# Optimization experiments

Hardware: AMD Instinct MI355X
Metric: run time of the kernel (lower is better)

## Reference

```python
import jax, jax.numpy as jnp
import numpy as np

B, C, F, N = 8, 128, 16, 512  # batch, in_channels, frames, num_nodes


def setup_inputs() -> dict:
    key = jax.random.key(0)
    k = jax.random.split(key, 6)
    return {
        # uniform(0,1) -> all entries nonzero -> complete graph with self-loops
        "Y": jax.random.uniform(k[0], (B, F, N, N), dtype=jnp.float32),
        "infos": jax.random.normal(k[1], (B, C, F, N), dtype=jnp.float32),
        # denseLayer: Linear(3C, C) -> weight [C, 3C], bias [C]
        "W_dense": jax.random.normal(k[2], (C, 3 * C), dtype=jnp.float32) / np.sqrt(3 * C).astype(np.float32),
        "b_dense": jax.random.normal(k[3], (C,), dtype=jnp.float32) * 0.01,
        # NodeApplyModule linear: Linear(C, C)
        "W_node": jax.random.normal(k[4], (C, C), dtype=jnp.float32) / np.sqrt(C).astype(np.float32),
        "b_node": jax.random.normal(k[5], (C,), dtype=jnp.float32) * 0.01,
    }


def reference(Y, infos, W_dense, b_dense, W_node, b_node):
    Bs, Cs, Fs, Ns = infos.shape
    # graph_update: frame 0 uses Y[:,0], frames 1..11 use Y[:,1], frames >11 use Y[:,2]
    frames = jnp.arange(Fs)
    y_idx = jnp.where(frames == 0, 0, jnp.where(frames <= 11, 1, 2))
    M = (Y[:, y_idx] != 0).astype(infos.dtype)          # [B,F,N,N] adjacency mask (u->v)
    X = jnp.transpose(infos, (0, 2, 3, 1))               # [B,F,N,C] node features

    # msg(u,v) = X[u] * (cat[X[u], X[v], X[u]-X[v]] @ W_dense.T + b_dense)
    # Linear is separable: gate(u,v) = S[u] + D[v] + b_dense with
    #   S = X @ (W1+W3).T, D = X @ (W2-W3).T
    W1, W2, W3 = jnp.split(W_dense, 3, axis=1)           # each [C,C]
    S = jnp.einsum('bfnc,dc->bfnd', X, W1 + W3)
    D = jnp.einsum('bfnc,dc->bfnd', X, W2 - W3)

    # mean over incoming edges u of msg(u,v):
    #   sum_u M[u,v] * X[u]*S[u]  +  (sum_u M[u,v]*X[u]) * (D[v]+b)
    A1 = jnp.einsum('bfuv,bfuc->bfvc', M, X * S)
    A2 = jnp.einsum('bfuv,bfuc->bfvc', M, X)
    deg = jnp.maximum(M.sum(axis=2), 1.0)[..., None]     # in-degree [B,F,N,1]
    agg = (A1 + A2 * (D + b_dense)) / deg

    # NodeApplyModule: relu(Linear(agg))
    h = jax.nn.relu(jnp.einsum('bfnc,oc->bfno', agg, W_node) + b_node)
    # reshape/permute to [B, C, F, N] and final relu (idempotent after relu)
    return jax.nn.relu(jnp.transpose(h, (0, 3, 1, 2)))
```

## Files before the change

### kernel.cpp

```cpp
#include <hip/hip_runtime.h>

#define B_ 8
#define C_ 128
#define F_ 16
#define N_ 512
#define CAP_ (N_ * N_)

typedef __attribute__((ext_vector_type(8))) short bf16x8;
typedef __attribute__((ext_vector_type(4))) float f32x4;

#define MFMA(a, b, c) __builtin_amdgcn_mfma_f32_16x16x32_bf16((a), (b), (c), 0, 0, 0)
#define SWZ(x) ((x) ^ ((((x) >> 8) & 7) << 4))

__device__ __forceinline__ ushort f2bf(float x) {
    unsigned u = __float_as_uint(x);
    u += 0x7fffu + ((u >> 16) & 1u);
    return (ushort)(u >> 16);
}

__global__ __launch_bounds__(256) void k_wprep(
    const float* __restrict__ Wd, const float* __restrict__ Wn,
    float* __restrict__ Wsum, float* __restrict__ Wdiff, float* __restrict__ WsumT,
    ushort* __restrict__ WdT_bf, float* __restrict__ WnT)
{
    int i = blockIdx.x * 256 + threadIdx.x;
    int d = i >> 7, c = i & 127;
    const float* row = Wd + (size_t)d * (3 * C_);
    float w1 = row[c], w2 = row[C_ + c], w3 = row[2 * C_ + c];
    float ws = w1 + w3, wdf = w2 - w3;
    Wsum[i] = ws;
    Wdiff[i] = wdf;
    WsumT[(size_t)c * C_ + d] = ws;
    WdT_bf[(size_t)c * C_ + d] = f2bf(wdf);
    WnT[i] = Wn[(size_t)(i & 127) * C_ + (i >> 7)];
}

__global__ __launch_bounds__(256) void k_deg(
    const float* __restrict__ Y, float* __restrict__ deg,
    int* __restrict__ cnt, int* __restrict__ list)
{
    __shared__ float red[256];
    int bg = blockIdx.x, vc = blockIdx.y, t = threadIdx.x;
    int b = bg / 3, g = bg % 3;
    int vl = t & 31, q = t >> 5;
    int v = vc * 32 + vl;
    const float* Yp = Y + ((size_t)b * F_ + g) * N_ * N_ + v;
    float dsum = 0.f;
    #pragma unroll 4
    for (int i = 0; i < 64; ++i) {
        int u = q * 64 + i;
        float a = Yp[(size_t)u * N_];
        if (a == 0.f) {
            int idx = atomicAdd(&cnt[bg], 1);
            list[(size_t)bg * CAP_ + idx] = (u << 9) | v;
        } else dsum += 1.f;
    }
    red[t] = dsum;
    __syncthreads();
    if (t < 32) {
        float s = 0.f;
        #pragma unroll
        for (int qq = 0; qq < 8; ++qq) s += red[qq * 32 + t];
        deg[(size_t)bg * N_ + vc * 32 + t] = s;
    }
}

__global__ __launch_bounds__(256) void k_gram(
    const float* __restrict__ infos, const float* __restrict__ WsumT,
    float* __restrict__ A1row, float* __restrict__ A2row)
{
    __shared__ float smf[8448];
    __shared__ float red[256];
    short* Xs = (short*)smf;
    float* Gl = smf;
    int bf = blockIdx.x, nh = blockIdx.y, t = threadIdx.x;
    int b = bf >> 4, f = bf & 15;
    const float* Xg = infos + ((size_t)b * C_ * F_ + f) * N_;

    float a2p0 = 0.f, a2p1 = 0.f, a2p2 = 0.f, a2p3 = 0.f;

    auto STAGE = [&](int buf, int ks) {
        int u0 = ks * 32;
        #pragma unroll
        for (int it = 0; it < 4; ++it) {
            int idx = it * 256 + t;
            int c = idx >> 3, uq = idx & 7;
            const float4 x = *(const float4*)(Xg + (size_t)c * (F_ * N_) + u0 + uq * 4);
            float s4 = x.x + x.y + x.z + x.w;
            if (it == 0) a2p0 += s4; else if (it == 1) a2p1 += s4;
            else if (it == 2) a2p2 += s4; else a2p3 += s4;
            short4 h;
            h.x = (short)f2bf(x.x); h.y = (short)f2bf(x.y);
            h.z = (short)f2bf(x.z); h.w = (short)f2bf(x.w);
            *(short4*)&Xs[buf * 5120 + c * 40 + uq * 4] = h;
        }
    };

    int l = t & 63, w = t >> 6;
    int r = l & 15, q = l >> 4;
    f32x4 acc[2][4];
    #pragma unroll
    for (int mi = 0; mi < 2; ++mi)
        #pragma unroll
        for (int ni = 0; ni < 4; ++ni) acc[mi][ni] = (f32x4){0.f, 0.f, 0.f, 0.f};

    STAGE(0, 0);
    for (int ks = 0; ks < 16; ++ks) {
        __syncthreads();
        if (ks < 15) STAGE((ks + 1) & 1, ks + 1);
        const short* Xb = &Xs[(ks & 1) * 5120];
        bf16x8 a0 = *(const bf16x8*)&Xb[(w * 32 + r) * 40 + q * 8];
        bf16x8 a1 = *(const bf16x8*)&Xb[(w * 32 + 16 + r) * 40 + q * 8];
        bf16x8 b0 = *(const bf16x8*)&Xb[(nh * 64 + 0  + r) * 40 + q * 8];
        bf16x8 b1 = *(const bf16x8*)&Xb[(nh * 64 + 16 + r) * 40 + q * 8];
        bf16x8 b2 = *(const bf16x8*)&Xb[(nh * 64 + 32 + r) * 40 + q * 8];
        bf16x8 b3 = *(const bf16x8*)&Xb[(nh * 64 + 48 + r) * 40 + q * 8];
        acc[0][0] = MFMA(a0, b0, acc[0][0]);
        acc[0][1] = MFMA(a0, b1, acc[0][1]);
        acc[0][2] = MFMA(a0, b2, acc[0][2]);
        acc[0][3] = MFMA(a0, b3, acc[0][3]);
        acc[1][0] = MFMA(a1, b0, acc[1][0]);
        acc[1][1] = MFMA(a1, b1, acc[1][1]);
        acc[1][2] = MFMA(a1, b2, acc[1][2]);
        acc[1][3] = MFMA(a1, b3, acc[1][3]);
    }
    __syncthreads();
    #pragma unroll
    for (int mi = 0; mi < 2; ++mi)
        #pragma unroll
        for (int ni = 0; ni < 4; ++ni) {
            int cb = w * 32 + mi * 16 + q * 4;
            int dl = ni * 16 + r;
            #pragma unroll
            for (int j = 0; j < 4; ++j) Gl[(cb + j) * 66 + dl] = acc[mi][ni][j];
        }
    __syncthreads();
    {
        int dl = t & 63, cq = t >> 6;
        float p = 0.f;
        #pragma unroll 8
        for (int i = 0; i < 32; ++i) {
            int c = cq * 32 + i;
            p += WsumT[(size_t)c * C_ + nh * 64 + dl] * Gl[c * 66 + dl];
        }
        red[t] = p;
    }
    __syncthreads();
    if (t < 64)
        A1row[(size_t)bf * C_ + nh * 64 + t] = red[t] + red[t + 64] + red[t + 128] + red[t + 192];
    if (nh == 0) {
        float vv0 = a2p0, vv1 = a2p1, vv2 = a2p2, vv3 = a2p3;
        #pragma unroll
        for (int it = 0; it < 4; ++it) {
            float v2 = (it == 0) ? vv0 : (it == 1) ? vv1 : (it == 2) ? vv2 : vv3;
            v2 += __shfl_xor(v2, 1);
            v2 += __shfl_xor(v2, 2);
            v2 += __shfl_xor(v2, 4);
            if ((t & 7) == 0) A2row[(size_t)bf * C_ + it * 32 + (t >> 3)] = v2;
        }
    }
}

__global__ __launch_bounds__(256) void k_meff(
    const float* __restrict__ A1row, const float* __restrict__ A2row,
    const float* __restrict__ Wn, const float* __restrict__ WnT,
    const ushort* __restrict__ WdT_bf, const float* __restrict__ bd,
    ushort* __restrict__ Meff_bf, float* __restrict__ c0all)
{
    __shared__ ushort Zl[16384];
    __shared__ ushort Wl[16384];
    __shared__ float A2l[C_], El[C_];
    int bf = blockIdx.x, t = threadIdx.x;
    if (t < C_) {
        float a2 = A2row[(size_t)bf * C_ + t];
        A2l[t] = a2;
        El[t] = A1row[(size_t)bf * C_ + t] + a2 * bd[t];
    }
    __syncthreads();
    #pragma unroll
    for (int it = 0; it < 8; ++it) {
        int idx = it * 256 + t;
        int rowi = idx >> 4, ch = idx & 15;
        bf16x8 wv = *(const bf16x8*)&WdT_bf[(size_t)rowi * C_ + ch * 8];
        *(bf16x8*)((char*)Wl + SWZ(rowi * 256 + ch * 16)) = wv;
        const float4 w0 = *(const float4*)&Wn[(size_t)rowi * C_ + ch * 8];
        const float4 w1 = *(const float4*)&Wn[(size_t)rowi * C_ + ch * 8 + 4];
        bf16x8 z;
        z[0] = (short)f2bf(w0.x * A2l[ch * 8 + 0]);
        z[1] = (short)f2bf(w0.y * A2l[ch * 8 + 1]);
        z[2] = (short)f2bf(w0.z * A2l[ch * 8 + 2]);
        z[3] = (short)f2bf(w0.w * A2l[ch * 8 + 3]);
        z[4] = (short)f2bf(w1.x * A2l[ch * 8 + 4]);
        z[5] = (short)f2bf(w1.y * A2l[ch * 8 + 5]);
        z[6] = (short)f2bf(w1.z * A2l[ch * 8 + 6]);
        z[7] = (short)f2bf(w1.w * A2l[ch * 8 + 7]);
        *(bf16x8*)((char*)Zl + SWZ(rowi * 256 + ch * 16)) = z;
    }
    __syncthreads();
    int l = t & 63, w = t >> 6, r = l & 15, q = l >> 4;
    f32x4 acc[2][8];
    #pragma unroll
    for (int mi = 0; mi < 2; ++mi)
        #pragma unroll
        for (int ni = 0; ni < 8; ++ni) acc[mi][ni] = (f32x4){0.f, 0.f, 0.f, 0.f};
    #pragma unroll
    for (int ks = 0; ks < 4; ++ks) {
        int ko = ks * 64 + q * 16;
        bf16x8 a0 = *(const bf16x8*)((char*)Zl + SWZ((w * 32 + r) * 256 + ko));
        bf16x8 a1 = *(const bf16x8*)((char*)Zl + SWZ((w * 32 + 16 + r) * 256 + ko));
        #pragma unroll
        for (int ni = 0; ni < 8; ++ni) {
            bf16x8 bb = *(const bf16x8*)((char*)Wl + SWZ((ni * 16 + r) * 256 + ko));
            acc[0][ni] = MFMA(a0, bb, acc[0][ni]);
            acc[1][ni] = MFMA(a1, bb, acc[1][ni]);
        }
    }
    __syncthreads();
    #pragma unroll
    for (int mi = 0; mi < 2; ++mi)
        #pragma unroll
        for (int ni = 0; ni < 8; ++ni) {
            int o = w * 32 + mi * 16 + q * 4;
            int c = ni * 16 + r;
            #pragma unroll
            for (int j = 0; j < 4; ++j) Zl[(o + j) * C_ + c] = f2bf(acc[mi][ni][j]);
        }
    __syncthreads();
    #pragma unroll
    for (int it = 0; it < 8; ++it) {
        int idx = it * 256 + t;
        int rowi = idx >> 4, ch = idx & 15;
        *(bf16x8*)&Meff_bf[(size_t)bf * 16384 + rowi * C_ + ch * 8] =
            *(const bf16x8*)&Zl[rowi * C_ + ch * 8];
    }
    if (t < C_) {
        float s = 0.f;
        for (int c = 0; c < C_; ++c) s += WnT[(size_t)c * C_ + t] * El[c];
        c0all[(size_t)bf * C_ + t] = s;
    }
}

__global__ __launch_bounds__(256) void k_final(
    const float* __restrict__ infos, const ushort* __restrict__ Meff_bf,
    const float* __restrict__ c0all, const float* __restrict__ deg,
    const int* __restrict__ cnt, const int* __restrict__ list,
    const float* __restrict__ Wsum, const float* __restrict__ Wdiff,
    const float* __restrict__ Wn, const float* __restrict__ bd, const float* __restrict__ bn,
    float* __restrict__ out)
{
    __shared__ ushort Ml[16384];
    __shared__ ushort Xv[8192];
    __shared__ float Xu[C_], Xvf[C_], NC[C_], corrv[C_];
    int bf = blockIdx.x, vb = blockIdx.y, t = threadIdx.x;
    int b = bf >> 4, f = bf & 15;
    int g = (f == 0) ? 0 : ((f <= 11) ? 1 : 2);
    int bg = b * 3 + g;
    int v0 = vb * 64;
    const float* Xg = infos + ((size_t)b * C_ * F_ + f) * N_;

    #pragma unroll
    for (int it = 0; it < 8; ++it) {
        int idx = it * 256 + t;
        int o = idx >> 4, ch = idx & 15;
        bf16x8 mv = *(const bf16x8*)&Meff_bf[(size_t)bf * 16384 + o * C_ + ch * 8];
        *(bf16x8*)((char*)Ml + SWZ(o * 256 + ch * 16)) = mv;
    }
    #pragma unroll
    for (int it = 0; it < 4; ++it) {
        int idx = it * 256 + t;
        int cp = idx >> 4, vq = idx & 15;
        const float* r0 = Xg + (size_t)(2 * cp) * (F_ * N_) + v0 + vq * 4;
        const float* r1 = r0 + (F_ * N_);
        float4 x0 = *(const float4*)r0;
        float4 x1 = *(const float4*)r1;
        float e0[4] = {x0.x, x0.y, x0.z, x0.w};
        float e1[4] = {x1.x, x1.y, x1.z, x1.w};
        #pragma unroll
        for (int j = 0; j < 4; ++j) {
            int vloc = vq * 4 + j;
            unsigned word = (unsigned)f2bf(e0[j]) | ((unsigned)f2bf(e1[j]) << 16);
            *(unsigned*)((char*)Xv + SWZ(vloc * 256 + cp * 4)) = word;
        }
    }
    __syncthreads();

    int l = t & 63, w = t >> 6, r = l & 15, q = l >> 4;
    f32x4 acc[2][4];
    #pragma unroll
    for (int mi = 0; mi < 2; ++mi)
        #pragma unroll
        for (int ni = 0; ni < 4; ++ni) acc[mi][ni] = (f32x4){0.f, 0.f, 0.f, 0.f};
    #pragma unroll
    for (int ks = 0; ks < 4; ++ks) {
        int ko = ks * 64 + q * 16;
        bf16x8 a0 = *(const bf16x8*)((char*)Ml + SWZ((w * 32 + r) * 256 + ko));
        bf16x8 a1 = *(const bf16x8*)((char*)Ml + SWZ((w * 32 + 16 + r) * 256 + ko));
        #pragma unroll
        for (int nt = 0; nt < 4; ++nt) {
            bf16x8 bb = *(const bf16x8*)((char*)Xv + SWZ((nt * 16 + r) * 256 + ko));
            acc[0][nt] = MFMA(a0, bb, acc[0][nt]);
            acc[1][nt] = MFMA(a1, bb, acc[1][nt]);
        }
    }

    int nz = cnt[bg];
    for (int e = 0; e < nz; ++e) {
        int p = list[(size_t)bg * CAP_ + e];
        int u = p >> 9, v = p & 511;
        if ((v >> 6) != vb) continue;
        int vloc = v - v0;
        __syncthreads();
        if (t < C_) {
            Xu[t]  = Xg[(size_t)t * (F_ * N_) + u];
            Xvf[t] = Xg[(size_t)t * (F_ * N_) + v];
        }
        __syncthreads();
        if (t < C_) {
            float s = 0.f, dv = 0.f;
            const float* wsr = Wsum + (size_t)t * C_;
            const float* wdr = Wdiff + (size_t)t * C_;
            for (int c = 0; c < C_; ++c) { s += wsr[c] * Xu[c]; dv += wdr[c] * Xvf[c]; }
            NC[t] = Xu[t] * (s + dv + bd[t]);
        }
        __syncthreads();
        if (t < C_) {
            float s = 0.f;
            const float* wnr = Wn + (size_t)t * C_;
            for (int c = 0; c < C_; ++c) s += wnr[c] * NC[c];
            corrv[t] = s;
        }
        __syncthreads();
        int ntv = vloc >> 4;
        #pragma unroll
        for (int nt = 0; nt < 4; ++nt) {
            if (nt == ntv && r == (vloc & 15)) {
                #pragma unroll
                for (int mi = 0; mi < 2; ++mi)
                    #pragma unroll
                    for (int j = 0; j < 4; ++j)
                        acc[mi][nt][j] -= corrv[w * 32 + mi * 16 + q * 4 + j];
            }
        }
    }

    float c0v[2][4], bnv[2][4];
    #pragma unroll
    for (int mi = 0; mi < 2; ++mi)
        #pragma unroll
        for (int j = 0; j < 4; ++j) {
            int o = w * 32 + mi * 16 + q * 4 + j;
            c0v[mi][j] = c0all[(size_t)bf * C_ + o];
            bnv[mi][j] = bn[o];
        }
    #pragma unroll
    for (int nt = 0; nt < 4; ++nt) {
        int v = v0 + nt * 16 + r;
        float dg = fmaxf(deg[(size_t)bg * N_ + v], 1.f);
        #pragma unroll
        for (int mi = 0; mi < 2; ++mi) {
            #pragma unroll
            for (int j = 0; j < 4; ++j) {
                int o = w * 32 + mi * 16 + q * 4 + j;
                float val = fmaxf((acc[mi][nt][j] + c0v[mi][j]) / dg + bnv[mi][j], 0.f);
                out[((size_t)b * C_ + o) * (F_ * N_) + (size_t)f * N_ + v] = val;
            }
        }
    }
}

extern "C" void kernel_launch(void* const* d_in, const int* in_sizes, int n_in,
                              void* d_out, int out_size, void* d_ws, size_t ws_size,
                              hipStream_t stream)
{
    const float* Y     = (const float*)d_in[0];
    const float* infos = (const float*)d_in[1];
    const float* Wd    = (const float*)d_in[2];
    const float* bd    = (const float*)d_in[3];
    const float* Wn    = (const float*)d_in[4];
    const float* bn    = (const float*)d_in[5];
    float* out = (float*)d_out;
    float* ws  = (float*)d_ws;

    float*  deg     = ws;
    int*    cnt     = (int*)(ws + 12288);
    float*  A1row   = ws + 12320;
    float*  A2row   = A1row + 16384;
    float*  Wsum    = A2row + 16384;
    float*  Wdiff   = Wsum + 16384;
    float*  WsumT   = Wdiff + 16384;
    float*  WnT     = WsumT + 16384;
    float*  c0all   = WnT + 16384;
    ushort* WdT_bf  = (ushort*)(c0all + 16384);
    ushort* Meff_bf = (ushort*)(c0all + 16384 + 8192);
    int*    list    = (int*)(c0all + 16384 + 8192 + 1048576);

    hipMemsetAsync(cnt, 0, 32 * sizeof(int), stream);
    k_wprep<<<64, 256, 0, stream>>>(Wd, Wn, Wsum, Wdiff, WsumT, WdT_bf, WnT);
    k_deg<<<dim3(24, 16), 256, 0, stream>>>(Y, deg, cnt, list);
    k_gram<<<dim3(B_ * F_, 2), 256, 0, stream>>>(infos, WsumT, A1row, A2row);
    k_meff<<<B_ * F_, 256, 0, stream>>>(A1row, A2row, Wn, WnT, WdT_bf, bd, Meff_bf, c0all);
    k_final<<<dim3(B_ * F_, 8), 256, 0, stream>>>(infos, Meff_bf, c0all, deg, cnt, list,
                                                  Wsum, Wdiff, Wn, bd, bn, out);
}
```

Measured before the change: 299.5 us.

## Fuse weight prep into degree kernel, prefetch gram tiles, coalesce final stores

After: 284.1 us. 1.05x faster.

```diff
diff --git a/kernel.cpp b/kernel.cpp
--- a/kernel.cpp
+++ b/kernel.cpp
@@ -1,4 +1,5 @@
 #include <hip/hip_runtime.h>
+#include <hip/hip_bf16.h>
 
 #define B_ 8
 #define C_ 128
@@ -13,55 +14,61 @@
 #define SWZ(x) ((x) ^ ((((x) >> 8) & 7) << 4))
 
 __device__ __forceinline__ ushort f2bf(float x) {
-    unsigned u = __float_as_uint(x);
-    u += 0x7fffu + ((u >> 16) & 1u);
-    return (ushort)(u >> 16);
-}
-
-__global__ __launch_bounds__(256) void k_wprep(
-    const float* __restrict__ Wd, const float* __restrict__ Wn,
+    union { __hip_bfloat16 h; ushort u; } cv;
+    cv.h = __float2bfloat16(x);
+    return cv.u;
+}
+
+__global__ __launch_bounds__(256) void k_prep(
+    const float* __restrict__ Y, const float* __restrict__ Wd, const float* __restrict__ Wn,
+    float* __restrict__ deg, int* __restrict__ cnt, int* __restrict__ list,
     float* __restrict__ Wsum, float* __restrict__ Wdiff, float* __restrict__ WsumT,
     ushort* __restrict__ WdT_bf, float* __restrict__ WnT)
 {
-    int i = blockIdx.x * 256 + threadIdx.x;
-    int d = i >> 7, c = i & 127;
-    const float* row = Wd + (size_t)d * (3 * C_);
-    float w1 = row[c], w2 = row[C_ + c], w3 = row[2 * C_ + c];
-    float ws = w1 + w3, wdf = w2 - w3;
-    Wsum[i] = ws;
-    Wdiff[i] = wdf;
-    WsumT[(size_t)c * C_ + d] = ws;
-    WdT_bf[(size_t)c * C_ + d] = f2bf(wdf);
-    WnT[i] = Wn[(size_t)(i & 127) * C_ + (i >> 7)];
-}
-
-__global__ __launch_bounds__(256) void k_deg(
-    const float* __restrict__ Y, float* __restrict__ deg,
-    int* __restrict__ cnt, int* __restrict__ list)
-{
-    __shared__ float red[256];
-    int bg = blockIdx.x, vc = blockIdx.y, t = threadIdx.x;
+    int t = threadIdx.x;
+    if (blockIdx.y == 8) {
+        for (int i = blockIdx.x * 256 + t; i < C_ * C_; i += 24 * 256) {
+            int d = i >> 7, c = i & 127;
+            const float* row = Wd + (size_t)d * (3 * C_);
+            float w1 = row[c], w2 = row[C_ + c], w3 = row[2 * C_ + c];
+            float ws = w1 + w3, wdf = w2 - w3;
+            Wsum[i] = ws;
+            Wdiff[i] = wdf;
+            WsumT[(size_t)c * C_ + d] = ws;
+            WdT_bf[(size_t)c * C_ + d] = f2bf(wdf);
+            WnT[i] = Wn[(size_t)(i & 127) * C_ + (i >> 7)];
+        }
+        return;
+    }
+    __shared__ float red0[256], red1[256];
+    int bg = blockIdx.x, vc = blockIdx.y;
     int b = bg / 3, g = bg % 3;
-    int vl = t & 31, q = t >> 5;
-    int v = vc * 32 + vl;
-    const float* Yp = Y + ((size_t)b * F_ + g) * N_ * N_ + v;
-    float dsum = 0.f;
+    int p = t & 31, q = t >> 5;
+    int v = vc * 64 + p * 2;
+    const float* Yp = Y + ((size_t)b * F_ + g) * N_ * N_;
+    float d0 = 0.f, d1 = 0.f;
     #pragma unroll 4
     for (int i = 0; i < 64; ++i) {
         int u = q * 64 + i;
-        float a = Yp[(size_t)u * N_];
-        if (a == 0.f) {
+        float2 a = *(const float2*)(Yp + (size_t)u * N_ + v);
+        if (a.x == 0.f) {
             int idx = atomicAdd(&cnt[bg], 1);
             list[(size_t)bg * CAP_ + idx] = (u << 9) | v;
-        } else dsum += 1.f;
-    }
-    red[t] = dsum;
+        } else d0 += 1.f;
+        if (a.y == 0.f) {
+            int idx = atomicAdd(&cnt[bg], 1);
+            list[(size_t)bg * CAP_ + idx] = (u << 9) | (v + 1);
+        } else d1 += 1.f;
+    }
+    red0[t] = d0;
+    red1[t] = d1;
     __syncthreads();
     if (t < 32) {
-        float s = 0.f;
-        #pragma unroll
-        for (int qq = 0; qq < 8; ++qq) s += red[qq * 32 + t];
-        deg[(size_t)bg * N_ + vc * 32 + t] = s;
+        float s0 = 0.f, s1 = 0.f;
+        #pragma unroll
+        for (int qq = 0; qq < 8; ++qq) { s0 += red0[qq * 32 + t]; s1 += red1[qq * 32 + t]; }
+        deg[(size_t)bg * N_ + vc * 64 + t * 2]     = s0;
+        deg[(size_t)bg * N_ + vc * 64 + t * 2 + 1] = s1;
     }
 }
 
@@ -78,21 +85,30 @@
     const float* Xg = infos + ((size_t)b * C_ * F_ + f) * N_;
 
     float a2p0 = 0.f, a2p1 = 0.f, a2p2 = 0.f, a2p3 = 0.f;
-
-    auto STAGE = [&](int buf, int ks) {
+    float4 pre0, pre1, pre2, pre3;
+    int sc = t >> 3, suq = t & 7;
+
+    auto LOADREG = [&](int ks) {
         int u0 = ks * 32;
+        const float* pbase = Xg + (size_t)sc * (F_ * N_) + u0 + suq * 4;
+        pre0 = *(const float4*)(pbase);
+        pre1 = *(const float4*)(pbase + 32 * (F_ * N_));
+        pre2 = *(const float4*)(pbase + 64 * (F_ * N_));
+        pre3 = *(const float4*)(pbase + 96 * (F_ * N_));
+    };
+    auto WRITELDS = [&](int buf) {
+        short* dst = &Xs[buf * 5120 + sc * 40 + suq * 4];
+        float4 xs[4] = {pre0, pre1, pre2, pre3};
         #pragma unroll
         for (int it = 0; it < 4; ++it) {
-            int idx = it * 256 + t;
-            int c = idx >> 3, uq = idx & 7;
-            const float4 x = *(const float4*)(Xg + (size_t)c * (F_ * N_) + u0 + uq * 4);
+            float4 x = xs[it];
             float s4 = x.x + x.y + x.z + x.w;
             if (it == 0) a2p0 += s4; else if (it == 1) a2p1 += s4;
             else if (it == 2) a2p2 += s4; else a2p3 += s4;
             short4 h;
             h.x = (short)f2bf(x.x); h.y = (short)f2bf(x.y);
             h.z = (short)f2bf(x.z); h.w = (short)f2bf(x.w);
-            *(short4*)&Xs[buf * 5120 + c * 40 + uq * 4] = h;
+            *(short4*)(dst + it * 32 * 40) = h;
         }
     };
 
@@ -104,10 +120,11 @@
         #pragma unroll
         for (int ni = 0; ni < 4; ++ni) acc[mi][ni] = (f32x4){0.f, 0.f, 0.f, 0.f};
 
-    STAGE(0, 0);
+    LOADREG(0);
+    WRITELDS(0);
     for (int ks = 0; ks < 16; ++ks) {
         __syncthreads();
-        if (ks < 15) STAGE((ks + 1) & 1, ks + 1);
+        if (ks < 15) LOADREG(ks + 1);
         const short* Xb = &Xs[(ks & 1) * 5120];
         bf16x8 a0 = *(const bf16x8*)&Xb[(w * 32 + r) * 40 + q * 8];
         bf16x8 a1 = *(const bf16x8*)&Xb[(w * 32 + 16 + r) * 40 + q * 8];
@@ -123,6 +140,7 @@
         acc[1][1] = MFMA(a1, b1, acc[1][1]);
         acc[1][2] = MFMA(a1, b2, acc[1][2]);
         acc[1][3] = MFMA(a1, b3, acc[1][3]);
+        if (ks < 15) WRITELDS((ks + 1) & 1);
     }
     __syncthreads();
     #pragma unroll
@@ -137,22 +155,21 @@
     __syncthreads();
     {
         int dl = t & 63, cq = t >> 6;
-        float p = 0.f;
+        float pacc = 0.f;
         #pragma unroll 8
         for (int i = 0; i < 32; ++i) {
             int c = cq * 32 + i;
-            p += WsumT[(size_t)c * C_ + nh * 64 + dl] * Gl[c * 66 + dl];
-        }
-        red[t] = p;
+            pacc += WsumT[(size_t)c * C_ + nh * 64 + dl] * Gl[c * 66 + dl];
+        }
+        red[t] = pacc;
     }
     __syncthreads();
     if (t < 64)
         A1row[(size_t)bf * C_ + nh * 64 + t] = red[t] + red[t + 64] + red[t + 128] + red[t + 192];
     if (nh == 0) {
-        float vv0 = a2p0, vv1 = a2p1, vv2 = a2p2, vv3 = a2p3;
         #pragma unroll
         for (int it = 0; it < 4; ++it) {
-            float v2 = (it == 0) ? vv0 : (it == 1) ? vv1 : (it == 2) ? vv2 : vv3;
+            float v2 = (it == 0) ? a2p0 : (it == 1) ? a2p1 : (it == 2) ? a2p2 : a2p3;
             v2 += __shfl_xor(v2, 1);
             v2 += __shfl_xor(v2, 2);
             v2 += __shfl_xor(v2, 4);
@@ -248,8 +265,10 @@
     const float* __restrict__ Wn, const float* __restrict__ bd, const float* __restrict__ bn,
     float* __restrict__ out)
 {
-    __shared__ ushort Ml[16384];
-    __shared__ ushort Xv[8192];
+    __shared__ char arena[49152];
+    ushort* Ml = (ushort*)arena;
+    ushort* Xv = (ushort*)(arena + 32768);
+    float*  Sl = (float*)arena;
     __shared__ float Xu[C_], Xvf[C_], NC[C_], corrv[C_];
     int bf = blockIdx.x, vb = blockIdx.y, t = threadIdx.x;
     int b = bf >> 4, f = bf & 15;
@@ -352,19 +371,29 @@
             c0v[mi][j] = c0all[(size_t)bf * C_ + o];
             bnv[mi][j] = bn[o];
         }
+    __syncthreads();
     #pragma unroll
     for (int nt = 0; nt < 4; ++nt) {
         int v = v0 + nt * 16 + r;
         float dg = fmaxf(deg[(size_t)bg * N_ + v], 1.f);
         #pragma unroll
         for (int mi = 0; mi < 2; ++mi) {
+            int o = w * 32 + mi * 16 + q * 4;
             #pragma unroll
             for (int j = 0; j < 4; ++j) {
-                int o = w * 32 + mi * 16 + q * 4 + j;
                 float val = fmaxf((acc[mi][nt][j] + c0v[mi][j]) / dg + bnv[mi][j], 0.f);
-                out[((size_t)b * C_ + o) * (F_ * N_) + (size_t)f * N_ + v] = val;
+                Sl[(o + j) * 66 + nt * 16 + r] = val;
             }
         }
+    }
+    __syncthreads();
+    {
+        int o = t >> 1, half = t & 1;
+        float* src = &Sl[o * 66 + half * 32];
+        float* dst = &out[((size_t)b * C_ + o) * (F_ * N_) + (size_t)f * N_ + v0 + half * 32];
+        #pragma unroll
+        for (int j = 0; j < 8; ++j)
+            *(float4*)(dst + j * 4) = *(const float4*)(src + j * 4);
     }
 }
 
@@ -395,8 +424,8 @@
     int*    list    = (int*)(c0all + 16384 + 8192 + 1048576);
 
     hipMemsetAsync(cnt, 0, 32 * sizeof(int), stream);
-    k_wprep<<<64, 256, 0, stream>>>(Wd, Wn, Wsum, Wdiff, WsumT, WdT_bf, WnT);
-    k_deg<<<dim3(24, 16), 256, 0, stream>>>(Y, deg, cnt, list);
+    k_prep<<<dim3(24, 9), 256, 0, stream>>>(Y, Wd, Wn, deg, cnt, list,
+                                            Wsum, Wdiff, WsumT, WdT_bf, WnT);
     k_gram<<<dim3(B_ * F_, 2), 256, 0, stream>>>(infos, WsumT, A1row, A2row);
     k_meff<<<B_ * F_, 256, 0, stream>>>(A1row, A2row, Wn, WnT, WdT_bf, bd, Meff_bf, c0all);
     k_final<<<dim3(B_ * F_, 8), 256, 0, stream>>>(infos, Meff_bf, c0all, deg, cnt, list,
```
